# Kernel optimization log

Measured on AMD Instinct MI355X. Metric: run time of the kernel, lower is better.

The kernel has to match this reference:

```python
import jax, jax.numpy as jnp
import numpy as np

B, N, NONGT, D, H, PE = 128, 36, 36, 1024, 16, 64
DG = D // H  # per-head dim = 64


def setup_inputs() -> dict:
    key = jax.random.key(0)
    ks = jax.random.split(key, 10)
    s = 0.02
    return {
        "roi_feat": jax.random.normal(ks[0], (B, N, D), jnp.float32),
        "adj_matrix": jax.random.randint(ks[1], (B, N, NONGT), 0, 2, jnp.int32),
        "position_embedding": jax.random.normal(ks[2], (B, N, NONGT, PE), jnp.float32),
        "label_biases_att": jax.random.normal(ks[3], (B, N, NONGT), jnp.float32) * 0.1,
        # effective (weight-normed) linear weights
        "Wq": jax.random.normal(ks[4], (D, D), jnp.float32) * s,
        "bq": jnp.zeros((D,), jnp.float32),
        "Wk": jax.random.normal(ks[5], (D, D), jnp.float32) * s,
        "bk": jnp.zeros((D,), jnp.float32),
        "Wpos": jax.random.normal(ks[6], (H, PE), jnp.float32) * s,
        "bpos": jnp.zeros((H,), jnp.float32),
        # grouped 1x1 conv (groups=H): per-head projection feat_dim -> feat_dim/H
        "Wout": jax.random.normal(ks[7], (H, DG, D), jnp.float32) * s,
        "bout": jnp.zeros((D,), jnp.float32),
    }


def reference(roi_feat, adj_matrix, position_embedding, label_biases_att,
              Wq, bq, Wk, bk, Wpos, bpos, Wout, bout):
    b, n, d = roi_feat.shape
    nongt = adj_matrix.shape[2]
    dg = d // H
    v = roi_feat[:, :nongt, :]                                  # [B,nongt,D]
    q = (roi_feat @ Wq.T + bq).reshape(b, n, H, dg)             # [B,N,H,dg]
    k = (v @ Wk.T + bk).reshape(b, nongt, H, dg)                # [B,nongt,H,dg]
    # scaled QK^T, laid out [B,N,H,nongt] (orig: matmul then transpose(1,2))
    aff = jnp.einsum('bnhd,bmhd->bnhm', q, k) / jnp.sqrt(jnp.float32(dg))
    # position log-bias
    pos = jax.nn.relu(position_embedding.reshape(b, n * nongt, -1) @ Wpos.T + bpos)
    pos = pos.reshape(b, n, nongt, H).transpose(0, 1, 3, 2)     # [B,N,H,nongt]
    waff = aff + jnp.log(jnp.maximum(pos, jnp.float32(1e-6)))
    # adjacency mask + label bias (orig does this in [B,N,nongt,H] layout; equivalent)
    mask = adj_matrix[:, :, None, :] > 0                        # [B,N,1,nongt]
    waff = jnp.where(mask, waff, jnp.float32(-9e15)) + label_biases_att[:, :, None, :]
    att = jax.nn.softmax(waff, axis=-1)                         # [B,N,H,nongt]
    # weighted sum of full V (note: V is full feat_dim per head, not dg)
    out_t = jnp.einsum('bnhm,bmd->bnhd', att, v)                # [B,N,H,D]
    # grouped 1x1 conv: per-head D -> D/H, heads concatenated
    out = jnp.einsum('bnhd,hed->bnhe', out_t, Wout).reshape(b, n, d) + bout
    return out
```

## Files before the change

kernel.cpp:

```cpp
#include <hip/hip_runtime.h>
#include <hip/hip_bf16.h>

#define BB 128
#define NN 36
#define DD 1024
#define HH 16
#define ROWS (BB*NN)

typedef __attribute__((ext_vector_type(8))) __bf16 bf16x8;
typedef __attribute__((ext_vector_type(4))) float f32x4;
typedef __attribute__((ext_vector_type(4))) unsigned short us4;

__device__ inline unsigned short f2bf(float f) {
    __hip_bfloat16 h = __float2bfloat16(f);
    return *reinterpret_cast<unsigned short*>(&h);
}

__device__ inline void async16(const unsigned short* g, unsigned short* l) {
    __builtin_amdgcn_global_load_lds((const __attribute__((address_space(1))) unsigned int*)g,
                                     (__attribute__((address_space(3))) unsigned int*)l, 16, 0, 0);
}

__global__ __launch_bounds__(256) void prep_kernel(const float* __restrict__ roi,
                                                   const float* __restrict__ Wq,
                                                   const float* __restrict__ Wk,
                                                   const float* __restrict__ Wout,
                                                   const float* __restrict__ pe,
                                                   const float* __restrict__ Wpos,
                                                   const float* __restrict__ bpos,
                                                   const int* __restrict__ adj,
                                                   const float* __restrict__ lbl,
                                                   unsigned short* __restrict__ roi_bf,
                                                   unsigned short* __restrict__ Wcat_bf,
                                                   float* __restrict__ extra) {
    const int bid = blockIdx.x, tid = threadIdx.x;
    if (bid < 4608) {
        int i = bid * 256 + tid;
        f32x4 v = ((const f32x4*)roi)[i];
        us4 o;
        o.x = f2bf(v[0]); o.y = f2bf(v[1]); o.z = f2bf(v[2]); o.w = f2bf(v[3]);
        ((us4*)roi_bf)[i] = o;
        return;
    }
    if (bid < 7680) {
        int wb = bid - 4608;
        int sel = wb >> 10;
        const float* src = sel == 0 ? Wq : (sel == 1 ? Wk : Wout);
        int i = (wb & 1023) * 256 + tid;
        f32x4 v = ((const f32x4*)src)[i];
        us4 o;
        o.x = f2bf(v[0]); o.y = f2bf(v[1]); o.z = f2bf(v[2]); o.w = f2bf(v[3]);
        ((us4*)(Wcat_bf + (size_t)sel * DD * DD))[i] = o;
        return;
    }
    __shared__ __align__(16) float wps[HH * 64];
    __shared__ float bps[HH];
    for (int i = tid; i < HH * 64; i += 256) wps[i] = Wpos[i];
    if (tid < HH) bps[tid] = bpos[tid];
    __syncthreads();

    int idx = (bid - 7680) * 256 + tid;
    f32x4 pr[16];
    const f32x4* pv = (const f32x4*)(pe + (size_t)idx * 64);
#pragma unroll
    for (int j = 0; j < 16; j++) pr[j] = pv[j];
    int a = adj[idx];
    float add = lbl[idx] + (a > 0 ? 0.f : -9e15f);
    int b = idx / 1296, nm = idx % 1296;
    size_t obase = (size_t)b * (16 * 1296) + nm;
    for (int hh = 0; hh < 16; hh++) {
        const f32x4* wv = (const f32x4*)(wps + hh * 64);
        f32x4 acc4 = {0.f, 0.f, 0.f, 0.f};
#pragma unroll
        for (int j = 0; j < 16; j++) acc4 += pr[j] * wv[j];
        float d = acc4[0] + acc4[1] + acc4[2] + acc4[3] + bps[hh];
        d = fmaxf(d, 0.f);
        d = __logf(fmaxf(d, 1e-6f));
        extra[obase + (size_t)hh * 1296] = d + add;
    }
}

__global__ __launch_bounds__(256, 2) void fused_kernel(const unsigned short* __restrict__ A,
                                                       const unsigned short* __restrict__ Wc,
                                                       const float* __restrict__ bq,
                                                       const float* __restrict__ bk,
                                                       const float* __restrict__ extra,
                                                       const float* __restrict__ bout,
                                                       float* __restrict__ out) {
    __shared__ __align__(16) unsigned short pool[29184];
    const int tid  = threadIdx.x;
    const int wave = tid >> 6, lane = tid & 63;
    const int quad = lane >> 4, l16 = lane & 15;
    const int h  = blockIdx.x & 15;
    const int bg = blockIdx.x >> 4;
    const int row0 = bg * 144;

    unsigned short* As = pool;
    unsigned short* Bs = pool + 9216;

    const unsigned short* gsrc[11];
    unsigned short* ldst[11];
#pragma unroll
    for (int i = 0; i < 11; i++) {
        int j = wave + 4 * i;
        int c = j * 64 + lane;
        if (j < 18) {
            int row = c >> 3;
            int col = ((c & 7) ^ (row & 7)) * 8;
            gsrc[i] = A + (size_t)(row0 + row) * DD + col;
            ldst[i] = As + j * 512;
        } else {
            int cb = c - 1152;
            int row = cb >> 3;
            int sec = row >> 6;
            int wrow = sec * DD + h * 64 + (row & 63);
            int col = ((cb & 7) ^ (row & 7)) * 8;
            gsrc[i] = Wc + (size_t)wrow * DD + col;
            ldst[i] = Bs + (j - 18) * 512;
        }
    }

    f32x4 acc[9][3] = {};

#pragma unroll
    for (int k0i = 0; k0i < 16; k0i++) {
#pragma unroll
        for (int i = 0; i < 11; i++) {
            if (i < 10 || wave < 2)
                async16(gsrc[i] + k0i * 64, ldst[i]);
        }
        __syncthreads();

#pragma unroll
        for (int ks = 0; ks < 2; ks++) {
            int kch = ks * 4 + quad;
            bf16x8 bfv[3], afv[9];
#pragma unroll
            for (int ct = 0; ct < 3; ct++) {
                int rowb = wave * 48 + ct * 16 + l16;
                bfv[ct] = *(const bf16x8*)&Bs[rowb * 64 + ((kch ^ (rowb & 7)) * 8)];
            }
#pragma unroll
            for (int rt = 0; rt < 9; rt++) {
                int rowa = rt * 16 + l16;
                afv[rt] = *(const bf16x8*)&As[rowa * 64 + ((kch ^ (rowa & 7)) * 8)];
            }
#pragma unroll
            for (int rt = 0; rt < 9; rt++)
#pragma unroll
                for (int ct = 0; ct < 3; ct++)
                    acc[rt][ct] = __builtin_amdgcn_mfma_f32_16x16x32_bf16(afv[rt], bfv[ct], acc[rt][ct], 0, 0, 0);
        }
        __syncthreads();
    }

    const int bat = wave;
    const float* exb = extra + ((size_t)((bg * 4 + bat) * 16 + h)) * 1296;
    float exv[3][4][3];
#pragma unroll
    for (int mt = 0; mt < 3; mt++)
#pragma unroll
        for (int r = 0; r < 4; r++) {
            int row = mt * 16 + quad * 4 + r;
#pragma unroll
            for (int nt = 0; nt < 3; nt++) {
                int col = nt * 16 + l16;
                exv[mt][r][nt] = (row < 36 && col < 36) ? exb[row * 36 + col] : 0.f;
            }
        }
    float bo[4];
#pragma unroll
    for (int nt = 0; nt < 4; nt++) bo[nt] = bout[h * 64 + nt * 16 + l16];

    unsigned short* qL = pool;
    unsigned short* kL = pool + 10368;
#pragma unroll
    for (int ct = 0; ct < 3; ct++) {
        int g = wave * 48 + ct * 16 + l16;
        int sec = g >> 6, e = g & 63;
        if (sec < 2) {
            unsigned short* dst = (sec == 0) ? qL : kL;
            float bias = (sec == 0) ? bq[h * 64 + e] : bk[h * 64 + e];
#pragma unroll
            for (int rt = 0; rt < 9; rt++)
#pragma unroll
                for (int r = 0; r < 4; r++) {
                    int row = rt * 16 + quad * 4 + r;
                    dst[row * 72 + e] = f2bf(acc[rt][ct][r] + bias);
                }
        }
    }
    __syncthreads();

    const unsigned short* qB = qL + bat * 36 * 72;
    const unsigned short* kB = kL + bat * 36 * 72;
    int rq[3];
#pragma unroll
    for (int t = 0; t < 3; t++) { int rr = t * 16 + l16; rq[t] = rr < 36 ? rr : 35; }

    f32x4 aff[3][3] = {};
#pragma unroll
    for (int ks = 0; ks < 2; ks++) {
        bf16x8 afr[3], bfr[3];
#pragma unroll
        for (int t = 0; t < 3; t++) afr[t] = *(const bf16x8*)&qB[rq[t] * 72 + ks * 32 + quad * 8];
#pragma unroll
        for (int t = 0; t < 3; t++) bfr[t] = *(const bf16x8*)&kB[rq[t] * 72 + ks * 32 + quad * 8];
#pragma unroll
        for (int mt = 0; mt < 3; mt++)
#pragma unroll
            for (int nt = 0; nt < 3; nt++)
                aff[mt][nt] = __builtin_amdgcn_mfma_f32_16x16x32_bf16(afr[mt], bfr[nt], aff[mt][nt], 0, 0, 0);
    }
    __syncthreads();

    unsigned short* vwT   = pool;
    unsigned short* attsL = pool + 18432 + bat * 2688;
#pragma unroll
    for (int mt = 0; mt < 3; mt++) {
#pragma unroll
        for (int r = 0; r < 4; r++) {
            int row = mt * 16 + quad * 4 + r;
            float w[3];
#pragma unroll
            for (int nt = 0; nt < 3; nt++) {
                int col = nt * 16 + l16;
                bool valid = (row < 36) && (col < 36);
                w[nt] = valid ? (aff[mt][nt][r] * 0.125f + exv[mt][r][nt]) : -3.4e38f;
            }
            float mx = fmaxf(fmaxf(w[0], w[1]), w[2]);
#pragma unroll
            for (int d = 1; d < 16; d <<= 1) mx = fmaxf(mx, __shfl_xor(mx, d));
            float e0 = __expf(w[0] - mx), e1 = __expf(w[1] - mx), e2 = __expf(w[2] - mx);
            float s = e0 + e1 + e2;
#pragma unroll
            for (int d = 1; d < 16; d <<= 1) s += __shfl_xor(s, d);
            float rs = 1.0f / s;
            attsL[row * 56 + 0  + l16] = f2bf(e0 * rs);
            attsL[row * 56 + 16 + l16] = f2bf(e1 * rs);
            attsL[row * 56 + 32 + l16] = f2bf(e2 * rs);
        }
    }
#pragma unroll
    for (int ct = 0; ct < 3; ct++) {
        int g = wave * 48 + ct * 16 + l16;
        int sec = g >> 6, e = g & 63;
        if (sec == 2) {
#pragma unroll
            for (int rt = 0; rt < 9; rt++)
#pragma unroll
                for (int r = 0; r < 4; r++) {
                    int row = rt * 16 + quad * 4 + r;
                    int bb = row / 36, m = row - bb * 36;
                    vwT[bb * 4608 + e * 72 + m] = f2bf(acc[rt][ct][r]);
                }
        }
    }
    {
        unsigned short* vB = vwT + bat * 4608;
        for (int m = 36; m < 64; m++) vB[lane * 72 + m] = 0;
    }
    __syncthreads();

    const unsigned short* vB = vwT + bat * 4608;
    f32x4 o[3][4] = {};
    {
        bf16x8 pa[3], pb[4];
#pragma unroll
        for (int mt = 0; mt < 3; mt++) pa[mt] = *(const bf16x8*)&attsL[(mt * 16 + l16) * 56 + quad * 8];
#pragma unroll
        for (int nt = 0; nt < 4; nt++) pb[nt] = *(const bf16x8*)&vB[(nt * 16 + l16) * 72 + quad * 8];
#pragma unroll
        for (int mt = 0; mt < 3; mt++)
#pragma unroll
            for (int nt = 0; nt < 4; nt++)
                o[mt][nt] = __builtin_amdgcn_mfma_f32_16x16x32_bf16(pa[mt], pb[nt], o[mt][nt], 0, 0, 0);
        bf16x8 zf = {};
#pragma unroll
        for (int mt = 0; mt < 3; mt++)
            pa[mt] = (quad < 2) ? *(const bf16x8*)&attsL[(mt * 16 + l16) * 56 + 32 + quad * 8] : zf;
#pragma unroll
        for (int nt = 0; nt < 4; nt++) pb[nt] = *(const bf16x8*)&vB[(nt * 16 + l16) * 72 + 32 + quad * 8];
#pragma unroll
        for (int mt = 0; mt < 3; mt++)
#pragma unroll
            for (int nt = 0; nt < 4; nt++)
                o[mt][nt] = __builtin_amdgcn_mfma_f32_16x16x32_bf16(pa[mt], pb[nt], o[mt][nt], 0, 0, 0);
    }

    const size_t obase = (size_t)((bg * 4 + bat) * 36) * DD + h * 64;
#pragma unroll
    for (int mt = 0; mt < 3; mt++)
#pragma unroll
        for (int r = 0; r < 4; r++) {
            int n = mt * 16 + quad * 4 + r;
            if (n < 36) {
#pragma unroll
                for (int nt = 0; nt < 4; nt++)
                    out[obase + (size_t)n * DD + nt * 16 + l16] = o[mt][nt][r] + bo[nt];
            }
        }
}

extern "C" void kernel_launch(void* const* d_in, const int* in_sizes, int n_in,
                              void* d_out, int out_size, void* d_ws, size_t ws_size,
                              hipStream_t stream) {
    const float* roi  = (const float*)d_in[0];
    const int*   adj  = (const int*)  d_in[1];
    const float* pe   = (const float*)d_in[2];
    const float* lbl  = (const float*)d_in[3];
    const float* Wq   = (const float*)d_in[4];
    const float* bq   = (const float*)d_in[5];
    const float* Wk   = (const float*)d_in[6];
    const float* bk   = (const float*)d_in[7];
    const float* Wpos = (const float*)d_in[8];
    const float* bpos = (const float*)d_in[9];
    const float* Wout = (const float*)d_in[10];
    const float* bout = (const float*)d_in[11];
    float* out = (float*)d_out;

    char* w = (char*)d_ws;
    unsigned short* roi_bf  = (unsigned short*)(w);
    unsigned short* Wcat_bf = (unsigned short*)(w + 9437184);
    float*          extra   = (float*)(w + 15728640);

    prep_kernel<<<8328, 256, 0, stream>>>(roi, Wq, Wk, Wout, pe, Wpos, bpos, adj, lbl,
                                          roi_bf, Wcat_bf, extra);
    fused_kernel<<<32 * 16, 256, 0, stream>>>(roi_bf, Wcat_bf, bq, bk, extra, bout, out);
}
```

Before: 170.6 us.

## Halve per-block batch tile to double grid size and raise occupancy

The fused kernel now processes 2 batches (72 rows) per block instead of 4, doubling the grid to 1024 blocks. Shared memory drops and launch bounds rise to 4 blocks per SM. The attention phase is split so two waves share each batch by M-tile rows. This targets better CU utilization on a 256-CU device, where 512 blocks left many CUs idle. The cost is that the weight slice is loaded twice as often, and the GEMM tile is padded from 72 to 80 rows.

```diff
diff --git a/kernel.cpp b/kernel.cpp
--- a/kernel.cpp
+++ b/kernel.cpp
@@ -80,73 +80,68 @@
     }
 }
 
-__global__ __launch_bounds__(256, 2) void fused_kernel(const unsigned short* __restrict__ A,
+__global__ __launch_bounds__(256, 4) void fused_kernel(const unsigned short* __restrict__ A,
                                                        const unsigned short* __restrict__ Wc,
                                                        const float* __restrict__ bq,
                                                        const float* __restrict__ bk,
                                                        const float* __restrict__ extra,
                                                        const float* __restrict__ bout,
                                                        float* __restrict__ out) {
-    __shared__ __align__(16) unsigned short pool[29184];
+    __shared__ __align__(16) unsigned short pool[17408];
     const int tid  = threadIdx.x;
     const int wave = tid >> 6, lane = tid & 63;
     const int quad = lane >> 4, l16 = lane & 15;
     const int h  = blockIdx.x & 15;
-    const int bg = blockIdx.x >> 4;
-    const int row0 = bg * 144;
-
-    unsigned short* As = pool;
-    unsigned short* Bs = pool + 9216;
-
-    const unsigned short* gsrc[11];
-    unsigned short* ldst[11];
-#pragma unroll
-    for (int i = 0; i < 11; i++) {
+    const int gb = blockIdx.x >> 4;
+    const int row0 = gb * 72;
+
+    const unsigned short* gsrc[9];
+#pragma unroll
+    for (int i = 0; i < 9; i++) {
         int j = wave + 4 * i;
         int c = j * 64 + lane;
-        if (j < 18) {
+        if (j < 10) {
             int row = c >> 3;
+            int rcl = row < 72 ? row : 71;
             int col = ((c & 7) ^ (row & 7)) * 8;
-            gsrc[i] = A + (size_t)(row0 + row) * DD + col;
-            ldst[i] = As + j * 512;
-        } else {
-            int cb = c - 1152;
+            gsrc[i] = A + (size_t)(row0 + rcl) * DD + col;
+        } else if (j < 34) {
+            int cb = c - 640;
             int row = cb >> 3;
             int sec = row >> 6;
             int wrow = sec * DD + h * 64 + (row & 63);
             int col = ((cb & 7) ^ (row & 7)) * 8;
             gsrc[i] = Wc + (size_t)wrow * DD + col;
-            ldst[i] = Bs + (j - 18) * 512;
-        }
-    }
-
-    f32x4 acc[9][3] = {};
+        } else gsrc[i] = A;
+    }
+
+    f32x4 acc[5][3] = {};
 
 #pragma unroll
     for (int k0i = 0; k0i < 16; k0i++) {
 #pragma unroll
-        for (int i = 0; i < 11; i++) {
-            if (i < 10 || wave < 2)
-                async16(gsrc[i] + k0i * 64, ldst[i]);
+        for (int i = 0; i < 9; i++) {
+            if (i < 8 || wave < 2)
+                async16(gsrc[i] + k0i * 64, pool + (wave + 4 * i) * 512);
         }
         __syncthreads();
 
 #pragma unroll
         for (int ks = 0; ks < 2; ks++) {
             int kch = ks * 4 + quad;
-            bf16x8 bfv[3], afv[9];
+            bf16x8 bfv[3], afv[5];
 #pragma unroll
             for (int ct = 0; ct < 3; ct++) {
                 int rowb = wave * 48 + ct * 16 + l16;
-                bfv[ct] = *(const bf16x8*)&Bs[rowb * 64 + ((kch ^ (rowb & 7)) * 8)];
-            }
-#pragma unroll
-            for (int rt = 0; rt < 9; rt++) {
+                bfv[ct] = *(const bf16x8*)&pool[5120 + rowb * 64 + ((kch ^ (rowb & 7)) * 8)];
+            }
+#pragma unroll
+            for (int rt = 0; rt < 5; rt++) {
                 int rowa = rt * 16 + l16;
-                afv[rt] = *(const bf16x8*)&As[rowa * 64 + ((kch ^ (rowa & 7)) * 8)];
-            }
-#pragma unroll
-            for (int rt = 0; rt < 9; rt++)
+                afv[rt] = *(const bf16x8*)&pool[rowa * 64 + ((kch ^ (rowa & 7)) * 8)];
+            }
+#pragma unroll
+            for (int rt = 0; rt < 5; rt++)
 #pragma unroll
                 for (int ct = 0; ct < 3; ct++)
                     acc[rt][ct] = __builtin_amdgcn_mfma_f32_16x16x32_bf16(afv[rt], bfv[ct], acc[rt][ct], 0, 0, 0);
@@ -154,18 +149,21 @@
         __syncthreads();
     }
 
-    const int bat = wave;
-    const float* exb = extra + ((size_t)((bg * 4 + bat) * 16 + h)) * 1296;
-    float exv[3][4][3];
-#pragma unroll
-    for (int mt = 0; mt < 3; mt++)
+    const int bat = wave & 1, sub = wave >> 1;
+    const int mt_base = sub ? 1 : 0, mt_cnt = sub ? 2 : 1;
+    const int b = gb * 2 + bat;
+
+    const float* exb = extra + ((size_t)(b * 16 + h)) * 1296;
+    float exv[2][4][3];
+#pragma unroll
+    for (int mi = 0; mi < 2; mi++)
 #pragma unroll
         for (int r = 0; r < 4; r++) {
-            int row = mt * 16 + quad * 4 + r;
+            int row = (mt_base + mi) * 16 + quad * 4 + r;
 #pragma unroll
             for (int nt = 0; nt < 3; nt++) {
                 int col = nt * 16 + l16;
-                exv[mt][r][nt] = (row < 36 && col < 36) ? exb[row * 36 + col] : 0.f;
+                exv[mi][r][nt] = (mi < mt_cnt && row < 36 && col < 36) ? exb[row * 36 + col] : 0.f;
             }
         }
     float bo[4];
@@ -173,7 +171,7 @@
     for (int nt = 0; nt < 4; nt++) bo[nt] = bout[h * 64 + nt * 16 + l16];
 
     unsigned short* qL = pool;
-    unsigned short* kL = pool + 10368;
+    unsigned short* kL = pool + 5184;
 #pragma unroll
     for (int ct = 0; ct < 3; ct++) {
         int g = wave * 48 + ct * 16 + l16;
@@ -182,11 +180,11 @@
             unsigned short* dst = (sec == 0) ? qL : kL;
             float bias = (sec == 0) ? bq[h * 64 + e] : bk[h * 64 + e];
 #pragma unroll
-            for (int rt = 0; rt < 9; rt++)
+            for (int rt = 0; rt < 5; rt++)
 #pragma unroll
                 for (int r = 0; r < 4; r++) {
                     int row = rt * 16 + quad * 4 + r;
-                    dst[row * 72 + e] = f2bf(acc[rt][ct][r] + bias);
+                    if (row < 72) dst[row * 72 + e] = f2bf(acc[rt][ct][r] + bias);
                 }
         }
     }
@@ -194,39 +192,43 @@
 
     const unsigned short* qB = qL + bat * 36 * 72;
     const unsigned short* kB = kL + bat * 36 * 72;
-    int rq[3];
-#pragma unroll
-    for (int t = 0; t < 3; t++) { int rr = t * 16 + l16; rq[t] = rr < 36 ? rr : 35; }
-
-    f32x4 aff[3][3] = {};
+    int rqa[2], rqb[3];
+#pragma unroll
+    for (int mi = 0; mi < 2; mi++) { int rr = (mt_base + mi) * 16 + l16; rqa[mi] = rr < 36 ? rr : 35; }
+#pragma unroll
+    for (int nt = 0; nt < 3; nt++) { int rr = nt * 16 + l16; rqb[nt] = rr < 36 ? rr : 35; }
+
+    f32x4 aff[2][3] = {};
 #pragma unroll
     for (int ks = 0; ks < 2; ks++) {
-        bf16x8 afr[3], bfr[3];
-#pragma unroll
-        for (int t = 0; t < 3; t++) afr[t] = *(const bf16x8*)&qB[rq[t] * 72 + ks * 32 + quad * 8];
-#pragma unroll
-        for (int t = 0; t < 3; t++) bfr[t] = *(const bf16x8*)&kB[rq[t] * 72 + ks * 32 + quad * 8];
-#pragma unroll
-        for (int mt = 0; mt < 3; mt++)
-#pragma unroll
-            for (int nt = 0; nt < 3; nt++)
-                aff[mt][nt] = __builtin_amdgcn_mfma_f32_16x16x32_bf16(afr[mt], bfr[nt], aff[mt][nt], 0, 0, 0);
+        bf16x8 afr[2], bfr[3];
+#pragma unroll
+        for (int mi = 0; mi < 2; mi++) afr[mi] = *(const bf16x8*)&qB[rqa[mi] * 72 + ks * 32 + quad * 8];
+#pragma unroll
+        for (int nt = 0; nt < 3; nt++) bfr[nt] = *(const bf16x8*)&kB[rqb[nt] * 72 + ks * 32 + quad * 8];
+#pragma unroll
+        for (int mi = 0; mi < 2; mi++)
+            if (mi < mt_cnt)
+#pragma unroll
+                for (int nt = 0; nt < 3; nt++)
+                    aff[mi][nt] = __builtin_amdgcn_mfma_f32_16x16x32_bf16(afr[mi], bfr[nt], aff[mi][nt], 0, 0, 0);
     }
     __syncthreads();
 
     unsigned short* vwT   = pool;
-    unsigned short* attsL = pool + 18432 + bat * 2688;
-#pragma unroll
-    for (int mt = 0; mt < 3; mt++) {
+    unsigned short* attsL = pool + 7168 + bat * 2688;
+#pragma unroll
+    for (int mi = 0; mi < 2; mi++) {
+        if (mi >= mt_cnt) continue;
 #pragma unroll
         for (int r = 0; r < 4; r++) {
-            int row = mt * 16 + quad * 4 + r;
+            int row = (mt_base + mi) * 16 + quad * 4 + r;
             float w[3];
 #pragma unroll
             for (int nt = 0; nt < 3; nt++) {
                 int col = nt * 16 + l16;
                 bool valid = (row < 36) && (col < 36);
-                w[nt] = valid ? (aff[mt][nt][r] * 0.125f + exv[mt][r][nt]) : -3.4e38f;
+                w[nt] = valid ? (aff[mi][nt][r] * 0.125f + exv[mi][r][nt]) : -3.4e38f;
             }
             float mx = fmaxf(fmaxf(w[0], w[1]), w[2]);
 #pragma unroll
@@ -247,59 +249,65 @@
         int sec = g >> 6, e = g & 63;
         if (sec == 2) {
 #pragma unroll
-            for (int rt = 0; rt < 9; rt++)
+            for (int rt = 0; rt < 5; rt++)
 #pragma unroll
                 for (int r = 0; r < 4; r++) {
                     int row = rt * 16 + quad * 4 + r;
-                    int bb = row / 36, m = row - bb * 36;
-                    vwT[bb * 4608 + e * 72 + m] = f2bf(acc[rt][ct][r]);
+                    if (row < 72) {
+                        int bb = row / 36, m = row - bb * 36;
+                        vwT[bb * 3584 + e * 56 + m] = f2bf(acc[rt][ct][r]);
+                    }
                 }
         }
     }
+    for (int i = lane; i < 384; i += 64) {
+        int e = sub * 32 + i / 12, m = 36 + i % 12;
+        vwT[bat * 3584 + e * 56 + m] = 0;
+    }
+    __syncthreads();
+
+    const unsigned short* vB = vwT + bat * 3584;
+    f32x4 o[2][4] = {};
     {
-        unsigned short* vB = vwT + bat * 4608;
-        for (int m = 36; m < 64; m++) vB[lane * 72 + m] = 0;
-    }
-    __syncthreads();
-
-    const unsigned short* vB = vwT + bat * 4608;
-    f32x4 o[3][4] = {};
-    {
-        bf16x8 pa[3], pb[4];
-#pragma unroll
-        for (int mt = 0; mt < 3; mt++) pa[mt] = *(const bf16x8*)&attsL[(mt * 16 + l16) * 56 + quad * 8];
-#pragma unroll
-        for (int nt = 0; nt < 4; nt++) pb[nt] = *(const bf16x8*)&vB[(nt * 16 + l16) * 72 + quad * 8];
-#pragma unroll
-        for (int mt = 0; mt < 3; mt++)
-#pragma unroll
-            for (int nt = 0; nt < 4; nt++)
-                o[mt][nt] = __builtin_amdgcn_mfma_f32_16x16x32_bf16(pa[mt], pb[nt], o[mt][nt], 0, 0, 0);
-        bf16x8 zf = {};
-#pragma unroll
-        for (int mt = 0; mt < 3; mt++)
-            pa[mt] = (quad < 2) ? *(const bf16x8*)&attsL[(mt * 16 + l16) * 56 + 32 + quad * 8] : zf;
-#pragma unroll
-        for (int nt = 0; nt < 4; nt++) pb[nt] = *(const bf16x8*)&vB[(nt * 16 + l16) * 72 + 32 + quad * 8];
-#pragma unroll
-        for (int mt = 0; mt < 3; mt++)
-#pragma unroll
-            for (int nt = 0; nt < 4; nt++)
-                o[mt][nt] = __builtin_amdgcn_mfma_f32_16x16x32_bf16(pa[mt], pb[nt], o[mt][nt], 0, 0, 0);
-    }
-
-    const size_t obase = (size_t)((bg * 4 + bat) * 36) * DD + h * 64;
-#pragma unroll
-    for (int mt = 0; mt < 3; mt++)
+        bf16x8 pa[2], pb[4], zf = {};
+#pragma unroll
+        for (int mi = 0; mi < 2; mi++) pa[mi] = *(const bf16x8*)&attsL[((mt_base + mi) * 16 + l16) * 56 + quad * 8];
+#pragma unroll
+        for (int nt = 0; nt < 4; nt++) pb[nt] = *(const bf16x8*)&vB[(nt * 16 + l16) * 56 + quad * 8];
+#pragma unroll
+        for (int mi = 0; mi < 2; mi++)
+            if (mi < mt_cnt)
+#pragma unroll
+                for (int nt = 0; nt < 4; nt++)
+                    o[mi][nt] = __builtin_amdgcn_mfma_f32_16x16x32_bf16(pa[mi], pb[nt], o[mi][nt], 0, 0, 0);
+#pragma unroll
+        for (int mi = 0; mi < 2; mi++)
+            pa[mi] = (quad < 2) ? *(const bf16x8*)&attsL[((mt_base + mi) * 16 + l16) * 56 + 32 + quad * 8] : zf;
+#pragma unroll
+        for (int nt = 0; nt < 4; nt++)
+            pb[nt] = (quad < 2) ? *(const bf16x8*)&vB[(nt * 16 + l16) * 56 + 32 + quad * 8] : zf;
+#pragma unroll
+        for (int mi = 0; mi < 2; mi++)
+            if (mi < mt_cnt)
+#pragma unroll
+                for (int nt = 0; nt < 4; nt++)
+                    o[mi][nt] = __builtin_amdgcn_mfma_f32_16x16x32_bf16(pa[mi], pb[nt], o[mi][nt], 0, 0, 0);
+    }
+
+    const size_t obase = (size_t)(b * 36) * DD + h * 64;
+#pragma unroll
+    for (int mi = 0; mi < 2; mi++) {
+        if (mi >= mt_cnt) continue;
 #pragma unroll
         for (int r = 0; r < 4; r++) {
-            int n = mt * 16 + quad * 4 + r;
+            int n = (mt_base + mi) * 16 + quad * 4 + r;
             if (n < 36) {
 #pragma unroll
                 for (int nt = 0; nt < 4; nt++)
-                    out[obase + (size_t)n * DD + nt * 16 + l16] = o[mt][nt][r] + bo[nt];
-            }
-        }
+                    out[obase + (size_t)n * DD + nt * 16 + l16] = o[mi][nt][r] + bo[nt];
+            }
+        }
+    }
 }
 
 extern "C" void kernel_launch(void* const* d_in, const int* in_sizes, int n_in,
@@ -326,5 +334,5 @@
 
     prep_kernel<<<8328, 256, 0, stream>>>(roi, Wq, Wk, Wout, pe, Wpos, bpos, adj, lbl,
                                           roi_bf, Wcat_bf, extra);
-    fused_kernel<<<32 * 16, 256, 0, stream>>>(roi_bf, Wcat_bf, bq, bk, extra, bout, out);
-}
+    fused_kernel<<<64 * 16, 256, 0, stream>>>(roi_bf, Wcat_bf, bq, bk, extra, bout, out);
+}
```

Result: slower. 206.1 us (+20.8%).
